# Kernel tuning notes

Measured on AMD Instinct MI355X. Metric: run time of the kernel, lower is better.

## Reference

```python
import jax, jax.numpy as jnp
import numpy as np

DIM = 768
HIDDEN = 4 * DIM          # shared expert hidden
NUM_EXPERTS = 8
TOPK = 2
D_LOW = DIM // 4          # 192


def setup_inputs() -> dict:
    key = jax.random.key(0)
    ks = jax.random.split(key, 8)
    B, C, H, W = 8, DIM, 32, 32
    x = jax.random.normal(ks[0], (B, C, H, W), dtype=jnp.float32)
    # shared expert (1x1 convs == per-pixel linear)
    w1 = jax.random.normal(ks[1], (HIDDEN, DIM), dtype=jnp.float32) * 0.02
    b1 = jnp.zeros((HIDDEN,), dtype=jnp.float32)
    w2 = jax.random.normal(ks[2], (DIM, HIDDEN), dtype=jnp.float32) * 0.02
    b2 = jnp.zeros((DIM,), dtype=jnp.float32)
    # router params (torch Linear weight layout [out, in])
    w_down = jax.random.normal(ks[3], (NUM_EXPERTS * D_LOW, DIM), dtype=jnp.float32) * 0.02
    router_w = jax.random.normal(ks[4], (1, D_LOW), dtype=jnp.float32) * 0.02
    w_up = jax.random.normal(ks[5], (NUM_EXPERTS, D_LOW, DIM), dtype=jnp.float32) * 0.02
    return {"x": x, "w1": w1, "b1": b1, "w2": w2, "b2": b2,
            "w_down": w_down, "router_w": router_w, "w_up": w_up}


def _gelu(v):
    # torch nn.GELU default = exact erf variant
    return jax.nn.gelu(v, approximate=False)


def reference(x, w1, b1, w2, b2, w_down, router_w, w_up):
    B, C, H, W = x.shape
    # ---- shared expert: conv1x1 -> GELU -> conv1x1 ----
    h = jnp.einsum('bchw,oc->bohw', x, w1) + b1[None, :, None, None]
    shared = jnp.einsum('bohw,co->bchw', _gelu(h), w2) + b2[None, :, None, None]
    # ---- AoE router over tokens ----
    N = H * W
    x_flat = x.reshape(B, C, N).transpose(0, 2, 1).reshape(B * N, C)  # [T, C]
    feats = (x_flat @ w_down.T).reshape(-1, NUM_EXPERTS, D_LOW)       # [T, E, d_low]
    logits = jnp.einsum('ted,d->te', feats, router_w[0])              # [T, E]
    probs = jax.nn.softmax(logits, axis=-1)
    topk_w, topk_i = jax.lax.top_k(probs, TOPK)                       # [T, k]
    topk_w = topk_w / jnp.sum(topk_w, axis=-1, keepdims=True)
    sel = jnp.take_along_axis(feats, topk_i[:, :, None], axis=1)      # [T, k, d_low]
    act = _gelu(sel)
    sel_w_up = w_up[topk_i]                                           # [T, k, d_low, C]
    expert_out = jnp.einsum('tkd,tkdm->tkm', act, sel_w_up)           # [T, k, C]
    weighted = jnp.sum(expert_out * topk_w[:, :, None], axis=1)       # [T, C]
    # aux load-balance loss
    mean_prob = jnp.mean(probs, axis=0)
    one_hot = jnp.sum(jax.nn.one_hot(topk_i, NUM_EXPERTS, dtype=probs.dtype), axis=1)
    mean_load = jnp.mean(one_hot, axis=0)
    aux_loss = NUM_EXPERTS * jnp.sum(mean_prob * mean_load)
    aoe = weighted.reshape(B, N, C).transpose(0, 2, 1).reshape(B, C, H, W)
    return x + shared + aoe, aux_loss
```

## Files before the change

### kernel.cpp

```cpp
#include <hip/hip_runtime.h>
#include <cstdint>
#include <cmath>

#define DIM   768
#define HID   3072
#define NEXP  8
#define DLOW  192
#define NPB   1024
#define NTOK  8192
#define KD    1536
#define KCAT  4608

typedef unsigned short ushort_t;
typedef short   short8  __attribute__((ext_vector_type(8)));
typedef float   float4v __attribute__((ext_vector_type(4)));

__device__ inline ushort_t f2b(float f) {
    union { float f; unsigned int i; } v; v.f = f;
    unsigned int x = v.i;
    return (ushort_t)((x + 0x7fffu + ((x >> 16) & 1u)) >> 16);
}
__device__ inline float gelu_fast(float x) {
    const float z = 1.5957691216057308f * x * __builtin_fmaf(0.044715f * x, x, 1.0f);
    return x * __builtin_amdgcn_rcpf(1.0f + __expf(-z));
}

__device__ __forceinline__ void async_ld16(const ushort_t* g, ushort_t* l) {
    __builtin_amdgcn_global_load_lds(
        (const __attribute__((address_space(1))) void*)g,
        (__attribute__((address_space(3))) void*)l,
        16, 0, 0);
}

__global__ __launch_bounds__(512)
void gemm_in(const ushort_t* __restrict__ A, const ushort_t* __restrict__ B,
             ushort_t* __restrict__ Cb, const float* __restrict__ bias,
             const int* __restrict__ tokE, const float* __restrict__ tokW,
             const float* __restrict__ accbuf, float* __restrict__ outAux,
             int m_base)
{
    __shared__ __align__(16) ushort_t As[256 * 64];
    __shared__ __align__(16) ushort_t Bs[128 * 64];

    const int tid  = threadIdx.x;
    const int lane = tid & 63;
    const int wave = tid >> 6;
    const int quad = lane >> 4;
    const int l16  = lane & 15;
    const int wm   = (wave >> 1) * 64;
    const int wn   = (wave & 1) * 64;

    const int nwg = gridDim.x * gridDim.y;
    const int bid = blockIdx.y * gridDim.x + blockIdx.x;
    const int swz = (bid & 7) * (nwg >> 3) + (bid >> 3);
    const int m0  = (swz / gridDim.x) * 256;
    const int n0  = (swz % gridDim.x) * 128;

    float4v acc[4][4];
#pragma unroll
    for (int i = 0; i < 4; i++)
#pragma unroll
        for (int j = 0; j < 4; j++) acc[i][j] = (float4v)0.0f;

    const ushort_t* ga[4]; ushort_t* la[4];
#pragma unroll
    for (int j = 0; j < 4; j++) {
        const int f = j * 512 + tid;
        const int mm = f >> 3;
        const int gs = ((f & 7) ^ (mm & 7)) * 8;
        ga[j] = A + (size_t)(m0 + mm) * DIM + gs;
        la[j] = &As[f * 8];
    }
    const ushort_t* gb[2]; ushort_t* lb[2];
#pragma unroll
    for (int j = 0; j < 2; j++) {
        const int f = j * 512 + tid;
        const int mm = f >> 3;
        const int gs = ((f & 7) ^ (mm & 7)) * 8;
        gb[j] = B + (size_t)(n0 + mm) * DIM + gs;
        lb[j] = &Bs[f * 8];
    }

    const ushort_t* pa[2][4]; const ushort_t* pb[2][4];
#pragma unroll
    for (int kh = 0; kh < 2; kh++)
#pragma unroll
        for (int i = 0; i < 4; i++) {
            const int ra = wm + i * 16 + l16;
            pa[kh][i] = &As[ra * 64 + (((quad + 4 * kh) ^ (ra & 7)) * 8)];
            const int rb = wn + i * 16 + l16;
            pb[kh][i] = &Bs[rb * 64 + (((quad + 4 * kh) ^ (rb & 7)) * 8)];
        }

    for (int k0 = 0; k0 < DIM; k0 += 64) {
        __syncthreads();
#pragma unroll
        for (int j = 0; j < 4; j++) async_ld16(ga[j] + k0, la[j]);
#pragma unroll
        for (int j = 0; j < 2; j++) async_ld16(gb[j] + k0, lb[j]);
        __syncthreads();
#pragma unroll
        for (int kh = 0; kh < 2; kh++) {
            short8 af[4], bv[4];
#pragma unroll
            for (int i = 0; i < 4; i++) af[i] = *(const short8*)pa[kh][i];
#pragma unroll
            for (int i = 0; i < 4; i++) bv[i] = *(const short8*)pb[kh][i];
#pragma unroll
            for (int im = 0; im < 4; im++)
#pragma unroll
                for (int in = 0; in < 4; in++)
                    acc[im][in] = __builtin_amdgcn_mfma_f32_16x16x32_bf16(
                        af[im], bv[in], acc[im][in], 0, 0, 0);
        }
    }

    if (n0 < HID) {
#pragma unroll
        for (int in = 0; in < 4; in++) {
            const int col = n0 + wn + in * 16 + l16;
            const float bvv = bias[col];
#pragma unroll
            for (int im = 0; im < 4; im++) {
                const int rowl = m0 + wm + im * 16 + quad * 4;
#pragma unroll
                for (int r = 0; r < 4; r++)
                    Cb[(size_t)(rowl + r) * KCAT + col] =
                        f2b(gelu_fast(acc[im][in][r] + bvv));
            }
        }
        if (m_base == 0 && blockIdx.x == 0 && blockIdx.y == 0 && tid == 0) {
            float aux = 0.0f;
            for (int e = 0; e < 8; e++) aux += accbuf[e] * accbuf[8 + e];
            outAux[0] = aux * 8.0f / ((float)NTOK * (float)NTOK);
        }
    } else {
        int eidx[4];
#pragma unroll
        for (int in = 0; in < 4; in++)
            eidx[in] = (n0 + wn + in * 16 - HID) / DLOW;
#pragma unroll
        for (int im = 0; im < 4; im++) {
            const int rowl = m0 + wm + im * 16 + quad * 4;
#pragma unroll
            for (int r = 0; r < 4; r++) {
                const int g = m_base + rowl + r;
                const int e0 = tokE[2 * g], e1 = tokE[2 * g + 1];
                const float w0 = tokW[2 * g], w1 = tokW[2 * g + 1];
#pragma unroll
                for (int in = 0; in < 4; in++) {
                    const int col = n0 + wn + in * 16 + l16;
                    const float m = (eidx[in] == e0) ? w0
                                  : ((eidx[in] == e1) ? w1 : 0.0f);
                    Cb[(size_t)(rowl + r) * KCAT + col] =
                        f2b(gelu_fast(acc[im][in][r]) * m);
                }
            }
        }
    }
}

__global__ __launch_bounds__(256)
void gemm_out(const ushort_t* __restrict__ A, const ushort_t* __restrict__ B,
              float* __restrict__ out, const float* __restrict__ bias,
              const float* __restrict__ X, int m_base)
{
    __shared__ __align__(16) ushort_t As[64 * 64];
    __shared__ __align__(16) ushort_t Bs[96 * 64];

    const int tid  = threadIdx.x;
    const int lane = tid & 63;
    const int wave = tid >> 6;
    const int quad = lane >> 4;
    const int l16  = lane & 15;
    const int wm   = (wave >> 1) * 32;
    const int wn   = (wave & 1) * 48;

    const int nwg = gridDim.x * gridDim.y;
    const int bid = blockIdx.y * gridDim.x + blockIdx.x;
    const int swz = (bid & 7) * (nwg >> 3) + (bid >> 3);
    const int m0  = (swz / gridDim.x) * 64;
    const int n0  = (swz % gridDim.x) * 96;

    float4v acc[2][3];
#pragma unroll
    for (int i = 0; i < 2; i++)
#pragma unroll
        for (int j = 0; j < 3; j++) acc[i][j] = (float4v)0.0f;

    const ushort_t* ga[2]; ushort_t* la[2];
#pragma unroll
    for (int j = 0; j < 2; j++) {
        const int f = j * 256 + tid;
        const int mm = f >> 3;
        const int gs = ((f & 7) ^ (mm & 7)) * 8;
        ga[j] = A + (size_t)(m0 + mm) * KCAT + gs;
        la[j] = &As[f * 8];
    }
    const ushort_t* gb[3]; ushort_t* lb[3];
#pragma unroll
    for (int j = 0; j < 3; j++) {
        const int f = j * 256 + tid;
        const int mm = f >> 3;
        const int gs = ((f & 7) ^ (mm & 7)) * 8;
        gb[j] = B + (size_t)(n0 + mm) * KCAT + gs;
        lb[j] = &Bs[f * 8];
    }

    const ushort_t* pa[2][2]; const ushort_t* pb[2][3];
#pragma unroll
    for (int kh = 0; kh < 2; kh++) {
#pragma unroll
        for (int i = 0; i < 2; i++) {
            const int ra = wm + i * 16 + l16;
            pa[kh][i] = &As[ra * 64 + (((quad + 4 * kh) ^ (ra & 7)) * 8)];
        }
#pragma unroll
        for (int i = 0; i < 3; i++) {
            const int rb = wn + i * 16 + l16;
            pb[kh][i] = &Bs[rb * 64 + (((quad + 4 * kh) ^ (rb & 7)) * 8)];
        }
    }

    for (int k0 = 0; k0 < KCAT; k0 += 64) {
        __syncthreads();
#pragma unroll
        for (int j = 0; j < 2; j++) async_ld16(ga[j] + k0, la[j]);
#pragma unroll
        for (int j = 0; j < 3; j++) async_ld16(gb[j] + k0, lb[j]);
        __syncthreads();
#pragma unroll
        for (int kh = 0; kh < 2; kh++) {
            short8 af[2], bv[3];
#pragma unroll
            for (int i = 0; i < 2; i++) af[i] = *(const short8*)pa[kh][i];
#pragma unroll
            for (int i = 0; i < 3; i++) bv[i] = *(const short8*)pb[kh][i];
#pragma unroll
            for (int im = 0; im < 2; im++)
#pragma unroll
                for (int in = 0; in < 3; in++)
                    acc[im][in] = __builtin_amdgcn_mfma_f32_16x16x32_bf16(
                        af[im], bv[in], acc[im][in], 0, 0, 0);
        }
    }

#pragma unroll
    for (int in = 0; in < 3; in++) {
        const int col = n0 + wn + in * 16 + l16;
        const float bvv = bias[col];
#pragma unroll
        for (int im = 0; im < 2; im++) {
            const int grow = m_base + m0 + wm + im * 16 + quad * 4;
            const int bb = grow >> 10, nn = grow & 1023;
            const size_t base = ((size_t)bb * DIM + col) * NPB + nn;
            const float4 xv = *(const float4*)(X + base);
            float4 v;
            v.x = acc[im][in][0] + bvv + xv.x;
            v.y = acc[im][in][1] + bvv + xv.y;
            v.z = acc[im][in][2] + bvv + xv.z;
            v.w = acc[im][in][3] + bvv + xv.w;
            *(float4*)(out + base) = v;
        }
    }
}

#define NB_TX   6144
#define NB_WUP  1152
#define NB_W2   (DIM * HID / 4 / 256)
#define NB_WIN  (KCAT * DIM / 4 / 256)
#define NB_WEFF (NEXP * DIM / 256)
#define NB_PREP (NB_TX + NB_WUP + NB_W2 + NB_WIN + NB_WEFF)

__global__ __launch_bounds__(256)
void prep_all(const float* __restrict__ x,  ushort_t* __restrict__ XT,
              const float* __restrict__ wup, ushort_t* __restrict__ Wcat,
              const float* __restrict__ w2,  const float* __restrict__ w1,
              const float* __restrict__ wdn, ushort_t* __restrict__ Win,
              const float* __restrict__ rw,  float* __restrict__ Weff,
              float* __restrict__ accb)
{
    __shared__ ushort_t tile[32][33];
    const int tid = threadIdx.x;
    const int tx = tid & 31, ty = tid >> 5;
    int blk = blockIdx.x;

    if (blk < NB_TX) {
        const int bx = blk & 31;
        const int rest = blk >> 5;
        const int by = rest % 24, b = rest / 24;
        const int n0 = bx * 32, c0 = by * 32;
#pragma unroll
        for (int j = 0; j < 4; j++)
            tile[ty + 8 * j][tx] =
                f2b(x[((size_t)b * DIM + c0 + ty + 8 * j) * NPB + n0 + tx]);
        __syncthreads();
#pragma unroll
        for (int j = 0; j < 4; j++)
            XT[((size_t)b * NPB + n0 + ty + 8 * j) * DIM + c0 + tx] =
                tile[tx][ty + 8 * j];
        return;
    }
    blk -= NB_TX;
    if (blk < NB_WUP) {
        const int bx = blk % 24, by = blk / 24;
        const int c0 = bx * 32, k0 = by * 32;
#pragma unroll
        for (int j = 0; j < 4; j++)
            tile[ty + 8 * j][tx] =
                f2b(wup[(size_t)(k0 + ty + 8 * j) * DIM + c0 + tx]);
        __syncthreads();
#pragma unroll
        for (int j = 0; j < 4; j++)
            Wcat[(size_t)(c0 + ty + 8 * j) * KCAT + HID + k0 + tx] =
                tile[tx][ty + 8 * j];
        return;
    }
    blk -= NB_WUP;
    if (blk < NB_W2) {
        const int i = blk * 256 + tid;
        const int c = i / (HID / 4), h = (i % (HID / 4)) * 4;
        const float4 v = *(const float4*)(w2 + (size_t)c * HID + h);
        uint2 p;
        p.x = (unsigned)f2b(v.x) | ((unsigned)f2b(v.y) << 16);
        p.y = (unsigned)f2b(v.z) | ((unsigned)f2b(v.w) << 16);
        *(uint2*)(Wcat + (size_t)c * KCAT + h) = p;
        return;
    }
    blk -= NB_W2;
    if (blk < NB_WIN) {
        const int i = blk * 256 + tid;
        const int n1 = HID * DIM / 4;
        const float4 v = (i < n1) ? ((const float4*)w1)[i]
                                  : ((const float4*)wdn)[i - n1];
        uint2 p;
        p.x = (unsigned)f2b(v.x) | ((unsigned)f2b(v.y) << 16);
        p.y = (unsigned)f2b(v.z) | ((unsigned)f2b(v.w) << 16);
        ((uint2*)Win)[i] = p;
        return;
    }
    blk -= NB_WIN;
    {
        const int idx = blk * 256 + tid;
        const int e = idx / DIM, c = idx % DIM;
        float s = 0.0f;
        for (int d = 0; d < DLOW; d++)
            s += wdn[(size_t)(e * DLOW + d) * DIM + c] * rw[d];
        Weff[idx] = s;
        if (blk == 0 && tid < 16) accb[tid] = 0.0f;
    }
}

__global__ __launch_bounds__(256)
void router_kernel(const float* __restrict__ x, const float* __restrict__ Weff,
                   int* __restrict__ tokE, float* __restrict__ tokW,
                   float* __restrict__ accbuf)
{
    __shared__ float sW[NEXP * DIM];
    __shared__ float sAcc[16];
    const int tid = threadIdx.x;
    for (int i = tid; i < NEXP * DIM; i += 256) sW[i] = Weff[i];
    if (tid < 16) sAcc[tid] = 0.0f;
    __syncthreads();

    const int t = blockIdx.x * 256 + tid;
    const int b = t >> 10, n = t & 1023;
    const float* xb = x + (size_t)b * DIM * NPB + n;

    float lg[8];
#pragma unroll
    for (int e = 0; e < 8; e++) lg[e] = 0.0f;
#pragma unroll 8
    for (int c = 0; c < DIM; c++) {
        const float xv = xb[(size_t)c * NPB];
#pragma unroll
        for (int e = 0; e < 8; e++) lg[e] += xv * sW[e * DIM + c];
    }

    float mx = lg[0];
#pragma unroll
    for (int e = 1; e < 8; e++) mx = fmaxf(mx, lg[e]);
    float pr[8], s = 0.0f;
#pragma unroll
    for (int e = 0; e < 8; e++) { pr[e] = expf(lg[e] - mx); s += pr[e]; }
    const float inv = 1.0f / s;
#pragma unroll
    for (int e = 0; e < 8; e++) pr[e] *= inv;
    int e0 = 0;
#pragma unroll
    for (int e = 1; e < 8; e++) if (pr[e] > pr[e0]) e0 = e;
    int e1 = (e0 == 0) ? 1 : 0;
#pragma unroll
    for (int e = 0; e < 8; e++) if (e != e0 && pr[e] > pr[e1]) e1 = e;
    const float wsum = pr[e0] + pr[e1];
    tokE[2 * t + 0] = e0;  tokE[2 * t + 1] = e1;
    tokW[2 * t + 0] = pr[e0] / wsum;  tokW[2 * t + 1] = pr[e1] / wsum;

#pragma unroll
    for (int e = 0; e < 8; e++) atomicAdd(&sAcc[e], pr[e]);
    atomicAdd(&sAcc[8 + e0], 1.0f);
    atomicAdd(&sAcc[8 + e1], 1.0f);
    __syncthreads();
    if (tid < 16) atomicAdd(&accbuf[tid], sAcc[tid]);
}

extern "C" void kernel_launch(void* const* d_in, const int* in_sizes, int n_in,
                              void* d_out, int out_size, void* d_ws, size_t ws_size,
                              hipStream_t stream)
{
    (void)in_sizes; (void)n_in; (void)out_size;

    const float* x   = (const float*)d_in[0];
    const float* w1  = (const float*)d_in[1];
    const float* b1  = (const float*)d_in[2];
    const float* w2  = (const float*)d_in[3];
    const float* b2  = (const float*)d_in[4];
    const float* wdn = (const float*)d_in[5];
    const float* rw  = (const float*)d_in[6];
    const float* wup = (const float*)d_in[7];
    float* out = (float*)d_out;

    char* ws = (char*)d_ws;
    size_t off = 0;
    ushort_t* XTbf = (ushort_t*)(ws + off); off += (size_t)NTOK * DIM * 2;
    ushort_t* Win  = (ushort_t*)(ws + off); off += (size_t)KCAT * DIM * 2;
    ushort_t* Wcat = (ushort_t*)(ws + off); off += (size_t)DIM * KCAT * 2;
    float*    Weff = (float*)  (ws + off);  off += (size_t)NEXP * DIM * 4;
    int*      tokE = (int*)    (ws + off);  off += (size_t)NTOK * 2 * 4;
    float*    tokW = (float*)  (ws + off);  off += (size_t)NTOK * 2 * 4;
    float*    accb = (float*)  (ws + off);  off += 256;

    int chunk = NTOK / 4;
    if      (ws_size >= off + (size_t)NTOK * KCAT * 2)       chunk = NTOK;
    else if (ws_size >= off + (size_t)(NTOK / 2) * KCAT * 2) chunk = NTOK / 2;
    ushort_t* HU = (ushort_t*)(ws + off);

    prep_all<<<NB_PREP, 256, 0, stream>>>(x, XTbf, wup, Wcat, w2, w1, wdn,
                                          Win, rw, Weff, accb);
    router_kernel<<<NTOK / 256, 256, 0, stream>>>(x, Weff, tokE, tokW, accb);

    for (int c = 0; c < NTOK / chunk; c++) {
        const ushort_t* Ax = XTbf + (size_t)c * chunk * DIM;
        const int m_base = c * chunk;
        gemm_in<<<dim3(KCAT / 128, chunk / 256), 512, 0, stream>>>(
            Ax, Win, HU, b1, tokE, tokW, accb, out + (size_t)NTOK * DIM, m_base);
        gemm_out<<<dim3(DIM / 96, chunk / 64), 256, 0, stream>>>(
            HU, Wcat, out, b2, x, m_base);
    }
}
```

Before: 320.3 us.

## Enlarge gemm_out tile to 128x96 with 128-wide K steps; vectorize x transpose

gemm_out's M tile doubles to 128 rows, so each wave now computes a 64x48 sub-tile. Each iteration loads 128 of K into two LDS halves, which halves the number of barriers per K sweep and raises MFMA work per shared-memory load. Separately, the x-to-bf16 transpose in prep_all now uses 64x64 tiles with float4 reads and 16-byte packed writes instead of scalar 32x32 tiles. The trade-off is more registers and LDS per block, and gemm_out launches half as many blocks.

```diff
diff --git a/kernel.cpp b/kernel.cpp
--- a/kernel.cpp
+++ b/kernel.cpp
@@ -160,37 +160,37 @@
     }
 }
 
-__global__ __launch_bounds__(256)
+__global__ __launch_bounds__(256, 2)
 void gemm_out(const ushort_t* __restrict__ A, const ushort_t* __restrict__ B,
               float* __restrict__ out, const float* __restrict__ bias,
               const float* __restrict__ X, int m_base)
 {
-    __shared__ __align__(16) ushort_t As[64 * 64];
-    __shared__ __align__(16) ushort_t Bs[96 * 64];
+    __shared__ __align__(16) ushort_t As[2 * 128 * 64];
+    __shared__ __align__(16) ushort_t Bs[2 * 96 * 64];
 
     const int tid  = threadIdx.x;
     const int lane = tid & 63;
     const int wave = tid >> 6;
     const int quad = lane >> 4;
     const int l16  = lane & 15;
-    const int wm   = (wave >> 1) * 32;
+    const int wm   = (wave >> 1) * 64;
     const int wn   = (wave & 1) * 48;
 
     const int nwg = gridDim.x * gridDim.y;
     const int bid = blockIdx.y * gridDim.x + blockIdx.x;
     const int swz = (bid & 7) * (nwg >> 3) + (bid >> 3);
-    const int m0  = (swz / gridDim.x) * 64;
+    const int m0  = (swz / gridDim.x) * 128;
     const int n0  = (swz % gridDim.x) * 96;
 
-    float4v acc[2][3];
-#pragma unroll
-    for (int i = 0; i < 2; i++)
+    float4v acc[4][3];
+#pragma unroll
+    for (int i = 0; i < 4; i++)
 #pragma unroll
         for (int j = 0; j < 3; j++) acc[i][j] = (float4v)0.0f;
 
-    const ushort_t* ga[2]; ushort_t* la[2];
-#pragma unroll
-    for (int j = 0; j < 2; j++) {
+    const ushort_t* ga[4]; ushort_t* la[4];
+#pragma unroll
+    for (int j = 0; j < 4; j++) {
         const int f = j * 256 + tid;
         const int mm = f >> 3;
         const int gs = ((f & 7) ^ (mm & 7)) * 8;
@@ -207,11 +207,11 @@
         lb[j] = &Bs[f * 8];
     }
 
-    const ushort_t* pa[2][2]; const ushort_t* pb[2][3];
+    const ushort_t* pa[2][4]; const ushort_t* pb[2][3];
 #pragma unroll
     for (int kh = 0; kh < 2; kh++) {
 #pragma unroll
-        for (int i = 0; i < 2; i++) {
+        for (int i = 0; i < 4; i++) {
             const int ra = wm + i * 16 + l16;
             pa[kh][i] = &As[ra * 64 + (((quad + 4 * kh) ^ (ra & 7)) * 8)];
         }
@@ -222,26 +222,34 @@
         }
     }
 
-    for (int k0 = 0; k0 < KCAT; k0 += 64) {
-        __syncthreads();
-#pragma unroll
-        for (int j = 0; j < 2; j++) async_ld16(ga[j] + k0, la[j]);
-#pragma unroll
-        for (int j = 0; j < 3; j++) async_ld16(gb[j] + k0, lb[j]);
-        __syncthreads();
-#pragma unroll
-        for (int kh = 0; kh < 2; kh++) {
-            short8 af[2], bv[3];
-#pragma unroll
-            for (int i = 0; i < 2; i++) af[i] = *(const short8*)pa[kh][i];
-#pragma unroll
-            for (int i = 0; i < 3; i++) bv[i] = *(const short8*)pb[kh][i];
-#pragma unroll
-            for (int im = 0; im < 2; im++)
-#pragma unroll
-                for (int in = 0; in < 3; in++)
-                    acc[im][in] = __builtin_amdgcn_mfma_f32_16x16x32_bf16(
-                        af[im], bv[in], acc[im][in], 0, 0, 0);
+    for (int k0 = 0; k0 < KCAT; k0 += 128) {
+        __syncthreads();
+#pragma unroll
+        for (int j = 0; j < 4; j++) async_ld16(ga[j] + k0,      la[j]);
+#pragma unroll
+        for (int j = 0; j < 4; j++) async_ld16(ga[j] + k0 + 64, la[j] + 128 * 64);
+#pragma unroll
+        for (int j = 0; j < 3; j++) async_ld16(gb[j] + k0,      lb[j]);
+#pragma unroll
+        for (int j = 0; j < 3; j++) async_ld16(gb[j] + k0 + 64, lb[j] + 96 * 64);
+        __syncthreads();
+#pragma unroll
+        for (int kp = 0; kp < 2; kp++) {
+            const int ao = kp * 128 * 64, bo = kp * 96 * 64;
+#pragma unroll
+            for (int kh = 0; kh < 2; kh++) {
+                short8 af[4], bv[3];
+#pragma unroll
+                for (int i = 0; i < 4; i++) af[i] = *(const short8*)(pa[kh][i] + ao);
+#pragma unroll
+                for (int i = 0; i < 3; i++) bv[i] = *(const short8*)(pb[kh][i] + bo);
+#pragma unroll
+                for (int im = 0; im < 4; im++)
+#pragma unroll
+                    for (int in = 0; in < 3; in++)
+                        acc[im][in] = __builtin_amdgcn_mfma_f32_16x16x32_bf16(
+                            af[im], bv[in], acc[im][in], 0, 0, 0);
+            }
         }
     }
 
@@ -250,7 +258,7 @@
         const int col = n0 + wn + in * 16 + l16;
         const float bvv = bias[col];
 #pragma unroll
-        for (int im = 0; im < 2; im++) {
+        for (int im = 0; im < 4; im++) {
             const int grow = m_base + m0 + wm + im * 16 + quad * 4;
             const int bb = grow >> 10, nn = grow & 1023;
             const size_t base = ((size_t)bb * DIM + col) * NPB + nn;
@@ -265,7 +273,7 @@
     }
 }
 
-#define NB_TX   6144
+#define NB_TX   1536
 #define NB_WUP  1152
 #define NB_W2   (DIM * HID / 4 / 256)
 #define NB_WIN  (KCAT * DIM / 4 / 256)
@@ -281,24 +289,42 @@
               float* __restrict__ accb)
 {
     __shared__ ushort_t tile[32][33];
+    __shared__ __align__(16) ushort_t t2[64 * 68];
     const int tid = threadIdx.x;
     const int tx = tid & 31, ty = tid >> 5;
     int blk = blockIdx.x;
 
     if (blk < NB_TX) {
-        const int bx = blk & 31;
-        const int rest = blk >> 5;
-        const int by = rest % 24, b = rest / 24;
-        const int n0 = bx * 32, c0 = by * 32;
-#pragma unroll
-        for (int j = 0; j < 4; j++)
-            tile[ty + 8 * j][tx] =
-                f2b(x[((size_t)b * DIM + c0 + ty + 8 * j) * NPB + n0 + tx]);
-        __syncthreads();
-#pragma unroll
-        for (int j = 0; j < 4; j++)
-            XT[((size_t)b * NPB + n0 + ty + 8 * j) * DIM + c0 + tx] =
-                tile[tx][ty + 8 * j];
+        const int bx = blk & 15;
+        const int rest = blk >> 4;
+        const int by = rest % 12, b = rest / 12;
+        const int n0 = bx * 64, c0 = by * 64;
+#pragma unroll
+        for (int j = 0; j < 4; j++) {
+            const int idx = j * 256 + tid;
+            const int c = idx >> 4, q = idx & 15;
+            const float4 v = *(const float4*)(
+                x + ((size_t)b * DIM + c0 + c) * NPB + n0 + 4 * q);
+            uint2 p;
+            p.x = (unsigned)f2b(v.x) | ((unsigned)f2b(v.y) << 16);
+            p.y = (unsigned)f2b(v.z) | ((unsigned)f2b(v.w) << 16);
+            *(uint2*)&t2[c * 68 + 4 * q] = p;
+        }
+        __syncthreads();
+#pragma unroll
+        for (int j = 0; j < 2; j++) {
+            const int w = (tid >> 3) + 32 * j;
+            const int p = tid & 7;
+            ushort_t u[8];
+#pragma unroll
+            for (int cc = 0; cc < 8; cc++) u[cc] = t2[(8 * p + cc) * 68 + w];
+            uint4 o;
+            o.x = (unsigned)u[0] | ((unsigned)u[1] << 16);
+            o.y = (unsigned)u[2] | ((unsigned)u[3] << 16);
+            o.z = (unsigned)u[4] | ((unsigned)u[5] << 16);
+            o.w = (unsigned)u[6] | ((unsigned)u[7] << 16);
+            *(uint4*)&XT[((size_t)b * NPB + n0 + w) * DIM + c0 + 8 * p] = o;
+        }
         return;
     }
     blk -= NB_TX;
@@ -444,7 +470,7 @@
         const int m_base = c * chunk;
         gemm_in<<<dim3(KCAT / 128, chunk / 256), 512, 0, stream>>>(
             Ax, Win, HU, b1, tokE, tokW, accb, out + (size_t)NTOK * DIM, m_base);
-        gemm_out<<<dim3(DIM / 96, chunk / 64), 256, 0, stream>>>(
+        gemm_out<<<dim3(DIM / 96, chunk / 128), 256, 0, stream>>>(
             HU, Wcat, out, b2, x, m_base);
     }
 }
```

Result: faster. 307.3 us (-4.1%).
